# Kernel tuning notes

Measured on AMD Instinct MI355X. Metric: run time of the kernel, lower is better.

## Reference

```python
import jax, jax.numpy as jnp
import numpy as np

COMPRESSION = 2

def setup_inputs() -> dict:
    key = jax.random.key(0)
    k = jax.random.split(key, 5)
    B, H, W, C, Ci = 8, 56, 56, 256, 128
    return {
        "x": jax.random.normal(k[0], (B, H, W, C), dtype=jnp.float32),
        "w_theta": jax.random.normal(k[1], (C, Ci), dtype=jnp.float32) * (2.0 / C) ** 0.5,
        "w_phi": jax.random.normal(k[2], (C, Ci), dtype=jnp.float32) * (2.0 / C) ** 0.5,
        "w_g": jax.random.normal(k[3], (C, Ci), dtype=jnp.float32) * (2.0 / C) ** 0.5,
        "w_final": jax.random.normal(k[4], (Ci, C), dtype=jnp.float32) * (2.0 / Ci) ** 0.5,
    }

def _maxpool1d(z, pool):
    # z: [B, N, Ci]; non-overlapping max pool along N (Keras MaxPool1D default stride=pool)
    B, N, Ci = z.shape
    return z[:, : (N // pool) * pool].reshape(B, N // pool, pool, Ci).max(axis=2)

def reference(x, w_theta, w_phi, w_g, w_final):
    B, H, W, C = x.shape
    Ci = w_theta.shape[1]
    N = H * W
    xf = x.reshape(B, N, C)
    # 1x1 convs == per-position matmuls
    theta = xf @ w_theta                      # [B, N, Ci]
    phi = _maxpool1d(xf @ w_phi, COMPRESSION)  # [B, N/2, Ci]
    g = _maxpool1d(xf @ w_g, COMPRESSION)      # [B, N/2, Ci]
    f = jnp.einsum('bnc,bmc->bnm', theta, phi)  # [B, N, N/2]
    f = jax.nn.softmax(f, axis=-1)
    y = jnp.einsum('bnm,bmc->bnc', f, g)        # [B, N, Ci]
    z = y @ w_final                              # [B, N, C]
    return x + z.reshape(B, H, W, C)
```

## Files before the change

kernel.cpp:

```cpp
#include <hip/hip_runtime.h>

typedef _Float16 f16x8 __attribute__((ext_vector_type(8)));
typedef _Float16 f16x4 __attribute__((ext_vector_type(4)));
typedef short s16x4 __attribute__((ext_vector_type(4)));
typedef float f32x4 __attribute__((ext_vector_type(4)));

#define MFMA_K32(a, b, c) __builtin_amdgcn_mfma_f32_16x16x32_f16(a, b, c, 0, 0, 0)
#define MFMA_BF(a, b, c)  __builtin_amdgcn_mfma_f32_16x16x16bf16_1k(a, b, c, 0, 0, 0)
#define MFMA_F16(a, b, c) __builtin_amdgcn_mfma_f32_16x16x16f16(a, b, c, 0, 0, 0)


__device__ __forceinline__ f16x8 ld8f(const float* __restrict__ p) {
    f32x4 a = *(const f32x4*)p;
    f32x4 b = *(const f32x4*)(p + 4);
    f16x8 r;
    r[0] = (_Float16)a[0]; r[1] = (_Float16)a[1];
    r[2] = (_Float16)a[2]; r[3] = (_Float16)a[3];
    r[4] = (_Float16)b[0]; r[5] = (_Float16)b[1];
    r[6] = (_Float16)b[2]; r[7] = (_Float16)b[3];
    return r;
}
__device__ __forceinline__ unsigned f2bf_rne(float f) {
    unsigned u = __float_as_uint(f);
    return (u + 0x7FFFu + ((u >> 16) & 1u)) >> 16;
}
__device__ __forceinline__ int bfpack_rtz(float lo, float hi) {
    return (int)((__float_as_uint(hi) & 0xFFFF0000u) | (__float_as_uint(lo) >> 16));
}

__global__ __launch_bounds__(256) void k_prep(
    const float* __restrict__ wt, const float* __restrict__ wp,
    const float* __restrict__ wg, const float* __restrict__ wf,
    _Float16* __restrict__ wt_f, _Float16* __restrict__ wfT_f) {
    int i = blockIdx.x * 256 + threadIdx.x;
    if (i < 12288) {
        int w    = i >> 12;
        int rem  = i & 4095;
        int ctkc = rem >> 6;
        int l    = rem & 63;
        const float* src = (w == 0) ? wt : (w == 1) ? wp : wg;
        const float* s = src + ((ctkc & 7) * 32 + (l >> 4) * 8) * 128
                             + (ctkc >> 3) * 16 + (l & 15);
        f16x8 v;
#pragma unroll
        for (int jj = 0; jj < 8; ++jj) v[jj] = (_Float16)s[jj * 128];
        *(f16x8*)(wt_f + i * 8) = v;
    } else {
        int j    = i - 12288;
        int ct   = j >> 8;
        int rem  = j & 255;
        int qt   = rem >> 2;
        int kc2e = rem & 3;
        int col  = ct * 16 + (qt & 15);
        int qq   = qt >> 4;
        f16x8 v;
#pragma unroll
        for (int jp = 0; jp < 8; ++jp) {
            int Ci = (kc2e * 2 + (jp >> 2)) * 16 + qq * 4 + (jp & 3);
            v[jp] = (_Float16)wf[Ci * 256 + col];
        }
        *(f16x8*)(wfT_f + j * 8) = v;
    }
}

__global__ __launch_bounds__(256) void k_proj(
    const float* __restrict__ x,
    const _Float16* __restrict__ wt_f,
    _Float16* __restrict__ theta_f,
    _Float16* __restrict__ phi_f,
    short* __restrict__ g_f)
{
    const int w    = blockIdx.y;
    const int wave = threadIdx.x >> 6;
    const int lane = threadIdx.x & 63;
    const int q = lane >> 4, t = lane & 15;
    const int tt = blockIdx.x * 4 + wave;

    __shared__ __align__(16) _Float16 Wl[32768];
    {
        const _Float16* src = wt_f + w * 32768;
#pragma unroll
        for (int j = 0; j < 16; ++j) {
            const int o8 = (j * 256 + threadIdx.x) * 8;
            *(f16x8*)(Wl + o8) = *(const f16x8*)(src + o8);
        }
    }
    __syncthreads();

    const int mrow = tt * 16 + t;
    f16x8 af[8];
#pragma unroll
    for (int kc = 0; kc < 8; ++kc)
        af[kc] = ld8f(x + mrow * 256 + kc * 32 + q * 8);

    const f32x4 zero = {0.f, 0.f, 0.f, 0.f};
    f32x4 acc[8];
#pragma unroll
    for (int ct = 0; ct < 8; ++ct) acc[ct] = zero;

    if (w == 2) {
#pragma unroll
        for (int ct = 0; ct < 8; ++ct) {
            const _Float16* Wc = Wl + (ct * 8) * 512 + lane * 8;
#pragma unroll
            for (int kc = 0; kc < 8; ++kc)
                acc[ct] = MFMA_K32(af[kc], *(const f16x8*)(Wc + kc * 512), acc[ct]);
        }
    } else {
#pragma unroll
        for (int ct = 0; ct < 8; ++ct) {
            const _Float16* Wc = Wl + (ct * 8) * 512 + lane * 8;
#pragma unroll
            for (int kc = 0; kc < 8; ++kc)
                acc[ct] = MFMA_K32(*(const f16x8*)(Wc + kc * 512), af[kc], acc[ct]);
        }
    }

    if (w == 0) {
        _Float16* tb = theta_f + tt * 2048;
#pragma unroll
        for (int ct = 0; ct < 8; ++ct) {
            f16x4 v;
#pragma unroll
            for (int r = 0; r < 4; ++r) v[r] = (_Float16)acc[ct][r];
            const int off = (ct >> 1) * 512
                          + (((ct & 1) * 2 + (q >> 1)) * 16 + t) * 8 + 4 * (q & 1);
            *(f16x4*)(tb + off) = v;
        }
        return;
    }

    const int b     = tt / 196;
    const int tl    = tt - b * 196;
    const int chunk = tl >> 2;
    const int sub   = tl & 3;

    if (w == 1) {
        _Float16* pcb = phi_f + (b * 49 + chunk) * 4096;
#pragma unroll
        for (int ct = 0; ct < 8; ++ct) {
            f32x4 pm;
#pragma unroll
            for (int r = 0; r < 4; ++r)
                pm[r] = fmaxf(acc[ct][r], __shfl_xor(acc[ct][r], 1));
            if (!(t & 1)) {
                f16x4 v;
#pragma unroll
                for (int r = 0; r < 4; ++r) v[r] = (_Float16)pm[r];
                const int off = ((sub >> 1) * 4 + (ct >> 1)) * 512
                              + ((((ct & 1) * 2 + (q >> 1)) * 16)
                                 + (sub & 1) * 8 + (t >> 1)) * 8 + 4 * (q & 1);
                *(f16x4*)(pcb + off) = v;
            }
        }
    } else {
        const int h   = sub >> 1;
        short* gcb = g_f + (b * 49 + chunk) * 4096;
        const int qv  = (sub & 1) * 2 + (q >> 1);
        const int jj0 = (q & 1) * 2;
#pragma unroll
        for (int ct = 0; ct < 8; ++ct) {
            unsigned lo = f2bf_rne(fmaxf(acc[ct][0], acc[ct][1]));
            unsigned hi = f2bf_rne(fmaxf(acc[ct][2], acc[ct][3]));
            *(unsigned*)(gcb + (ct * 2 + h) * 256 + (qv * 16 + t) * 4 + jj0) = lo | (hi << 16);
        }
    }
}

__global__ __launch_bounds__(256) void k_attn(
    const _Float16* __restrict__ theta_f,
    const _Float16* __restrict__ phi_f,
    const short* __restrict__ g_f,
    const _Float16* __restrict__ wfT_f,
    const float* __restrict__ x,
    float* __restrict__ out)
{
    const int blk  = blockIdx.x;
    const int b    = blk & 7;
    const int blkm = blk >> 3;
    const int wave = threadIdx.x >> 6;
    const int lane = threadIdx.x & 63;
    const int q = lane >> 4, t = lane & 15;
    const int p = wave >> 1;
    const int h = wave & 1;

    __shared__ __align__(16) _Float16 kv[2][8192];
    __shared__ float lred[2][2][64];

    const int tIdx0 = b * 196 + blkm * 4;
    const _Float16* ph = phi_f + b * 200704;
    const _Float16* gt = (const _Float16*)(g_f + b * 200704);

    f16x8 qf[2][4];
#pragma unroll
    for (int m = 0; m < 2; ++m)
#pragma unroll
        for (int kc = 0; kc < 4; ++kc)
            qf[m][kc] = *(const f16x8*)(theta_f + (tIdx0 + 2 * p + m) * 2048 + kc * 512 + lane * 8);

    const f32x4 zero = {0.f, 0.f, 0.f, 0.f};
    f32x4 o[2][8];
#pragma unroll
    for (int m = 0; m < 2; ++m)
#pragma unroll
        for (int ct = 0; ct < 8; ++ct) o[m][ct] = zero;
    float lsum[2] = {0.f, 0.f};
    const float L2E = 1.44269504f, SHIFT = 104.0f;

    const _Float16* src0 = (wave < 2) ? (ph + wave * 2048) : (gt + (wave - 2) * 2048);
    const int doff = wave * 2048;

    f16x8 sr[4];
#pragma unroll
    for (int j = 0; j < 4; ++j)
        sr[j] = *(const f16x8*)(src0 + j * 512 + lane * 8);
#pragma unroll
    for (int j = 0; j < 4; ++j)
        *(f16x8*)(&kv[0][doff + j * 512 + lane * 8]) = sr[j];
    __syncthreads();

#pragma unroll 1
    for (int i = 0; i < 49; ++i) {
        if (i + 1 < 49) {
            const _Float16* s = src0 + (i + 1) * 4096;
#pragma unroll
            for (int j = 0; j < 4; ++j)
                sr[j] = *(const f16x8*)(s + j * 512 + lane * 8);
        }

        const _Float16* buf = &kv[i & 1][0];
        f32x4 st[2] = {zero, zero};
#pragma unroll
        for (int kc = 0; kc < 4; ++kc) {
            f16x8 a = *(const f16x8*)(buf + (h * 4 + kc) * 512 + lane * 8);
            st[0] = MFMA_K32(a, qf[0][kc], st[0]);
            st[1] = MFMA_K32(a, qf[1][kc], st[1]);
        }

        union { int i2[2]; s16x4 v; } u[2];
#pragma unroll
        for (int m = 0; m < 2; ++m) {
            f32x4 pv;
#pragma unroll
            for (int r = 0; r < 4; ++r)
                pv[r] = exp2f(st[m][r] * L2E - SHIFT);
            lsum[m] += (pv[0] + pv[1]) + (pv[2] + pv[3]);
            u[m].i2[0] = bfpack_rtz(pv[0], pv[1]);
            u[m].i2[1] = bfpack_rtz(pv[2], pv[3]);
        }

#pragma unroll
        for (int ct = 0; ct < 8; ++ct) {
            s16x4 vf = *(const s16x4*)(buf + 4096 + (ct * 2 + h) * 256 + lane * 4);
            o[0][ct] = MFMA_BF(vf, u[0].v, o[0][ct]);
            o[1][ct] = MFMA_BF(vf, u[1].v, o[1][ct]);
        }

        if (i + 1 < 49) {
            _Float16* d = &kv[(i + 1) & 1][doff];
#pragma unroll
            for (int j = 0; j < 4; ++j)
                *(f16x8*)(d + j * 512 + lane * 8) = sr[j];
        }
        __syncthreads();
    }

    float* cb = (float*)&kv[0][0];
    if (h == 1) {
#pragma unroll
        for (int m = 0; m < 2; ++m) {
#pragma unroll
            for (int ct = 0; ct < 8; ++ct)
                *(f32x4*)&cb[p * 4096 + (m * 8 + ct) * 256 + lane * 4] = o[m][ct];
            lred[p][m][lane] = lsum[m];
        }
    }
    __syncthreads();
    if (h == 0) {
#pragma unroll
        for (int m = 0; m < 2; ++m) {
#pragma unroll
            for (int ct = 0; ct < 8; ++ct)
                o[m][ct] += *(const f32x4*)&cb[p * 4096 + (m * 8 + ct) * 256 + lane * 4];
            lsum[m] += lred[p][m][lane];
        }
    }
    __syncthreads();
    if (h == 0) {
#pragma unroll
        for (int ct = 0; ct < 8; ++ct)
            *(f32x4*)&cb[p * 4096 + ct * 256 + lane * 4] = o[1][ct];
        lred[p][0][lane] = lsum[1];
    }
    __syncthreads();

    f32x4 ow[8];
    float lw;
    if (h == 0) {
#pragma unroll
        for (int ct = 0; ct < 8; ++ct) ow[ct] = o[0][ct];
        lw = lsum[0];
    } else {
#pragma unroll
        for (int ct = 0; ct < 8; ++ct)
            ow[ct] = *(const f32x4*)&cb[p * 4096 + ct * 256 + lane * 4];
        lw = lred[p][0][lane];
    }

    float lf = lw;
    lf += __shfl_xor(lf, 16);
    lf += __shfl_xor(lf, 32);
    const float inv = 1.0f / lf;

    f16x4 yf[8];
#pragma unroll
    for (int ct = 0; ct < 8; ++ct)
#pragma unroll
        for (int r = 0; r < 4; ++r)
            yf[ct][r] = (_Float16)(ow[ct][r] * inv);

    const int row = (tIdx0 + 2 * p + h) * 16 + t;
#pragma unroll 2
    for (int ctile = 0; ctile < 16; ++ctile) {
        union { f16x8 v8; f16x4 v4[2]; } w[4];
#pragma unroll
        for (int pp = 0; pp < 4; ++pp)
            w[pp].v8 = *(const f16x8*)(wfT_f + ctile * 2048 + lane * 32 + pp * 8);
        f32x4 acc = zero;
#pragma unroll
        for (int kc2 = 0; kc2 < 8; ++kc2)
            acc = MFMA_F16(w[kc2 >> 1].v4[kc2 & 1], yf[kc2], acc);
        const int col = ctile * 16 + q * 4;
        f32x4 xv = *(const f32x4*)(x + row * 256 + col);
        *(f32x4*)(out + row * 256 + col) = acc + xv;
    }
}

extern "C" void kernel_launch(void* const* d_in, const int* in_sizes, int n_in,
                              void* d_out, int out_size, void* d_ws, size_t ws_size,
                              hipStream_t stream) {
    const float* x  = (const float*)d_in[0];
    const float* wt = (const float*)d_in[1];
    const float* wp = (const float*)d_in[2];
    const float* wg = (const float*)d_in[3];
    const float* wf = (const float*)d_in[4];
    float* out = (float*)d_out;

    _Float16* ws      = (_Float16*)d_ws;
    _Float16* wt_f    = ws;
    _Float16* wfT_f   = ws + 98304;
    _Float16* theta_f = ws + 131072;
    _Float16* phi_f   = ws + 3342336;
    short*    g_f     = (short*)(ws + 4947968);

    k_prep<<<dim3(64),      256, 0, stream>>>(wt, wp, wg, wf, wt_f, wfT_f);
    k_proj<<<dim3(392, 3),  256, 0, stream>>>(x, wt_f, theta_f, phi_f, g_f);
    k_attn<<<dim3(392),     256, 0, stream>>>(theta_f, phi_f, g_f, wfT_f, x, out);
}
```

Measured before the change: 151.3 us.

## Halve query rows per attention block and double the grid for parallelism

Each attention block now handles 2 query tiles instead of 4. Each wave pair owns one 16-row tile, and the two halves split the output projection columns. The grid doubles from 392 to 784 blocks to fill more CUs and cut per-wave register pressure. In exchange, every block re-streams the full phi/g keys and values, which doubles K/V global traffic and the LDS staging work per query.

```diff
diff --git a/kernel.cpp b/kernel.cpp
--- a/kernel.cpp
+++ b/kernel.cpp
@@ -181,30 +181,26 @@
     const int wave = threadIdx.x >> 6;
     const int lane = threadIdx.x & 63;
     const int q = lane >> 4, t = lane & 15;
-    const int p = wave >> 1;
+    const int m = wave >> 1;
     const int h = wave & 1;
 
     __shared__ __align__(16) _Float16 kv[2][8192];
-    __shared__ float lred[2][2][64];
-
-    const int tIdx0 = b * 196 + blkm * 4;
+    __shared__ float lred[2][64];
+
+    const int tIdx0 = b * 196 + blkm * 2;
     const _Float16* ph = phi_f + b * 200704;
     const _Float16* gt = (const _Float16*)(g_f + b * 200704);
 
-    f16x8 qf[2][4];
-#pragma unroll
-    for (int m = 0; m < 2; ++m)
-#pragma unroll
-        for (int kc = 0; kc < 4; ++kc)
-            qf[m][kc] = *(const f16x8*)(theta_f + (tIdx0 + 2 * p + m) * 2048 + kc * 512 + lane * 8);
+    f16x8 qf[4];
+#pragma unroll
+    for (int kc = 0; kc < 4; ++kc)
+        qf[kc] = *(const f16x8*)(theta_f + (tIdx0 + m) * 2048 + kc * 512 + lane * 8);
 
     const f32x4 zero = {0.f, 0.f, 0.f, 0.f};
-    f32x4 o[2][8];
-#pragma unroll
-    for (int m = 0; m < 2; ++m)
-#pragma unroll
-        for (int ct = 0; ct < 8; ++ct) o[m][ct] = zero;
-    float lsum[2] = {0.f, 0.f};
+    f32x4 o[8];
+#pragma unroll
+    for (int ct = 0; ct < 8; ++ct) o[ct] = zero;
+    float lsum = 0.f;
     const float L2E = 1.44269504f, SHIFT = 104.0f;
 
     const _Float16* src0 = (wave < 2) ? (ph + wave * 2048) : (gt + (wave - 2) * 2048);
@@ -229,31 +225,26 @@
         }
 
         const _Float16* buf = &kv[i & 1][0];
-        f32x4 st[2] = {zero, zero};
+        f32x4 st = zero;
 #pragma unroll
         for (int kc = 0; kc < 4; ++kc) {
             f16x8 a = *(const f16x8*)(buf + (h * 4 + kc) * 512 + lane * 8);
-            st[0] = MFMA_K32(a, qf[0][kc], st[0]);
-            st[1] = MFMA_K32(a, qf[1][kc], st[1]);
-        }
-
-        union { int i2[2]; s16x4 v; } u[2];
-#pragma unroll
-        for (int m = 0; m < 2; ++m) {
-            f32x4 pv;
-#pragma unroll
-            for (int r = 0; r < 4; ++r)
-                pv[r] = exp2f(st[m][r] * L2E - SHIFT);
-            lsum[m] += (pv[0] + pv[1]) + (pv[2] + pv[3]);
-            u[m].i2[0] = bfpack_rtz(pv[0], pv[1]);
-            u[m].i2[1] = bfpack_rtz(pv[2], pv[3]);
-        }
+            st = MFMA_K32(a, qf[kc], st);
+        }
+
+        f32x4 pv;
+#pragma unroll
+        for (int r = 0; r < 4; ++r)
+            pv[r] = exp2f(st[r] * L2E - SHIFT);
+        lsum += (pv[0] + pv[1]) + (pv[2] + pv[3]);
+        union { int i2[2]; s16x4 v; } u;
+        u.i2[0] = bfpack_rtz(pv[0], pv[1]);
+        u.i2[1] = bfpack_rtz(pv[2], pv[3]);
 
 #pragma unroll
         for (int ct = 0; ct < 8; ++ct) {
             s16x4 vf = *(const s16x4*)(buf + 4096 + (ct * 2 + h) * 256 + lane * 4);
-            o[0][ct] = MFMA_BF(vf, u[0].v, o[0][ct]);
-            o[1][ct] = MFMA_BF(vf, u[1].v, o[1][ct]);
+            o[ct] = MFMA_BF(vf, u.v, o[ct]);
         }
 
         if (i + 1 < 49) {
@@ -268,46 +259,30 @@
     float* cb = (float*)&kv[0][0];
     if (h == 1) {
 #pragma unroll
-        for (int m = 0; m < 2; ++m) {
-#pragma unroll
-            for (int ct = 0; ct < 8; ++ct)
-                *(f32x4*)&cb[p * 4096 + (m * 8 + ct) * 256 + lane * 4] = o[m][ct];
-            lred[p][m][lane] = lsum[m];
-        }
+        for (int ct = 0; ct < 8; ++ct)
+            *(f32x4*)&cb[m * 2048 + ct * 256 + lane * 4] = o[ct];
+        lred[m][lane] = lsum;
     }
     __syncthreads();
     if (h == 0) {
 #pragma unroll
-        for (int m = 0; m < 2; ++m) {
-#pragma unroll
-            for (int ct = 0; ct < 8; ++ct)
-                o[m][ct] += *(const f32x4*)&cb[p * 4096 + (m * 8 + ct) * 256 + lane * 4];
-            lsum[m] += lred[p][m][lane];
-        }
+        for (int ct = 0; ct < 8; ++ct)
+            o[ct] += *(const f32x4*)&cb[m * 2048 + ct * 256 + lane * 4];
+        lsum += lred[m][lane];
+#pragma unroll
+        for (int ct = 0; ct < 8; ++ct)
+            *(f32x4*)&cb[m * 2048 + ct * 256 + lane * 4] = o[ct];
+        lred[m][lane] = lsum;
     }
     __syncthreads();
-    if (h == 0) {
+    if (h == 1) {
 #pragma unroll
         for (int ct = 0; ct < 8; ++ct)
-            *(f32x4*)&cb[p * 4096 + ct * 256 + lane * 4] = o[1][ct];
-        lred[p][0][lane] = lsum[1];
-    }
-    __syncthreads();
-
-    f32x4 ow[8];
-    float lw;
-    if (h == 0) {
-#pragma unroll
-        for (int ct = 0; ct < 8; ++ct) ow[ct] = o[0][ct];
-        lw = lsum[0];
-    } else {
-#pragma unroll
-        for (int ct = 0; ct < 8; ++ct)
-            ow[ct] = *(const f32x4*)&cb[p * 4096 + ct * 256 + lane * 4];
-        lw = lred[p][0][lane];
-    }
-
-    float lf = lw;
+            o[ct] = *(const f32x4*)&cb[m * 2048 + ct * 256 + lane * 4];
+        lsum = lred[m][lane];
+    }
+
+    float lf = lsum;
     lf += __shfl_xor(lf, 16);
     lf += __shfl_xor(lf, 32);
     const float inv = 1.0f / lf;
@@ -317,11 +292,12 @@
     for (int ct = 0; ct < 8; ++ct)
 #pragma unroll
         for (int r = 0; r < 4; ++r)
-            yf[ct][r] = (_Float16)(ow[ct][r] * inv);
-
-    const int row = (tIdx0 + 2 * p + h) * 16 + t;
+            yf[ct][r] = (_Float16)(o[ct][r] * inv);
+
+    const int row = (tIdx0 + m) * 16 + t;
 #pragma unroll 2
-    for (int ctile = 0; ctile < 16; ++ctile) {
+    for (int ci = 0; ci < 8; ++ci) {
+        const int ctile = h * 8 + ci;
         union { f16x8 v8; f16x4 v4[2]; } w[4];
 #pragma unroll
         for (int pp = 0; pp < 4; ++pp)
@@ -355,5 +331,5 @@
 
     k_prep<<<dim3(64),      256, 0, stream>>>(wt, wp, wg, wf, wt_f, wfT_f);
     k_proj<<<dim3(392, 3),  256, 0, stream>>>(x, wt_f, theta_f, phi_f, g_f);
-    k_attn<<<dim3(392),     256, 0, stream>>>(theta_f, phi_f, g_f, wfT_f, x, out);
-}
+    k_attn<<<dim3(784),     256, 0, stream>>>(theta_f, phi_f, g_f, wfT_f, x, out);
+}
```

Result: no change. 150.8 us (-0.3%).
